# Optimization experiments

Measured on AMD Instinct MI355X. Metric: run time of the kernel, lower is better.

## Reference

```python
import jax, jax.numpy as jnp
import numpy as np

ALPHA = 0.2          # LeakyReLU negative slope
NEG_CAP = -9e15      # clamp used by the original torch.where on log(adj)


def setup_inputs() -> dict:
    key = jax.random.key(0)
    B, C, V, L, H, E = 4, 32, 1000, 12, 4, 20000
    k1, k2, k3, k4 = jax.random.split(key, 4)
    x = jax.random.normal(k1, (B, C, V, L), dtype=jnp.float32)
    # xavier_uniform-like scale with gain 1.414 (use normal for simplicity of stats)
    W = jax.random.normal(k2, (H, C, C), dtype=jnp.float32) * np.float32(1.414 * np.sqrt(2.0 / (C + C)))
    a = jax.random.normal(k3, (H, 2 * C, 1), dtype=jnp.float32) * np.float32(1.414 * np.sqrt(2.0 / (2 * C + 1)))
    # edge list: V self-loops (every row nonempty -> rowsum > 0) + random edges
    rng = np.random.default_rng(0)
    src = np.concatenate([np.arange(V), rng.integers(0, V, E - V)]).astype(np.int64)
    dst = np.concatenate([np.arange(V), rng.integers(0, V, E - V)]).astype(np.int64)
    edge_index = jnp.asarray(np.stack([src, dst]))           # [2, E]
    # edge_val = adj[edge0, edge1]; positive so log() is finite
    edge_val = jax.random.uniform(k4, (E,), dtype=jnp.float32, minval=0.05, maxval=1.0)
    return {"x": x, "W": W, "a": a, "edge_index": edge_index, "edge_val": edge_val}


def reference(x, W, a, edge_index, edge_val):
    # x: [B,C,V,L], W: [H,C,C], a: [H,2C,1], edge_index: [2,E], edge_val: [E]
    H, C = W.shape[0], W.shape[2]
    V = x.shape[2]
    e0, e1 = edge_index[0], edge_index[1]

    # h = einsum('ncvl,hcd->hndvl'): [H,B,C,V,L]
    h = jnp.einsum('bcvl,hcd->hbdvl', x, W)

    # attention score: a applied to cat(h[src], h[dst]) == a_src.h[src] + a_dst.h[dst]
    a_src, a_dst = a[:, :C, 0], a[:, C:, 0]                   # [H,C]
    s_src = jnp.einsum('hbcvl,hc->hbvl', h, a_src)            # [H,B,V,L]
    s_dst = jnp.einsum('hbcvl,hc->hbvl', h, a_dst)
    score = s_src[:, :, e0, :] + s_dst[:, :, e1, :]           # [H,B,E,L]

    edge_e = jnp.exp(-jax.nn.leaky_relu(score, ALPHA))        # [H,B,E,L]
    lv = jnp.maximum(jnp.log(edge_val), NEG_CAP)              # [E]
    edge_e = edge_e * lv[None, None, :, None]
    # (dropout is identity in eval mode)

    # e_rowsum: sparse [V,V] @ ones -> per-row sum, scatter by e0: [V,H,B,L]
    rowsum = jax.ops.segment_sum(jnp.moveaxis(edge_e, 2, 0), e0, num_segments=V)

    # h_prime numerator: scatter (edge_e * h[dst]) by e0
    hg = h[:, :, :, e1, :]                                    # [H,B,C,E,L]
    msg = edge_e[:, :, None, :, :] * hg                       # [H,B,C,E,L]
    num = jax.ops.segment_sum(jnp.moveaxis(msg, 3, 0), e0, num_segments=V)  # [V,H,B,C,L]

    h_prime = num / rowsum[:, :, :, None, :]                  # [V,H,B,C,L]
    h_avg = jnp.mean(h_prime, axis=1)                         # [V,B,C,L]
    out = jnp.transpose(h_avg, (1, 2, 0, 3))                  # [B,C,V,L]
    return jax.nn.elu(out)
```

## Files before the change

### kernel.cpp

```cpp
#include <hip/hip_runtime.h>
#include <hip/hip_bf16.h>
#include <math.h>

#define HH 4
#define BB 4
#define CC 32
#define VV 1000
#define LL 12
#define EE 20000
#define NBL (BB * LL)
#define SS (HH * NBL)
#define RCAP 128
#define LALPHA 0.2f
#define NEG_CAP_F -9000000000000000.0f

typedef unsigned int uint;
typedef unsigned short ushort;

__global__ __launch_bounds__(256) void k_h(const float* __restrict__ x,
                                           const float* __restrict__ W,
                                           const float* __restrict__ a,
                                           ushort* __restrict__ h_g,
                                           float* __restrict__ s_src,
                                           float* __restrict__ s_dst,
                                           int* __restrict__ cnt) {
  if (blockIdx.y == 0 && blockIdx.x < 4) {
    cnt[blockIdx.x * 256 + threadIdx.x] = 0;
  }

  __shared__ float W_lds[HH * CC * CC];
  __shared__ float a_lds[HH * 2 * CC];
  __shared__ float x_lds[CC * 8 * LL];
  __shared__ float wa[HH][2][CC];
  const int tid = threadIdx.x;
  const int b = blockIdx.y;
  const int v0 = blockIdx.x * 8;

  for (int i = tid; i < HH * CC * CC; i += 256) W_lds[i] = W[i];
  a_lds[tid] = a[tid];
  for (int i = tid; i < CC * 8 * LL; i += 256) {
    int ci = i / (8 * LL);
    int r = i - ci * (8 * LL);
    x_lds[i] = x[(b * CC + ci) * (VV * LL) + v0 * LL + r];
  }
  __syncthreads();

  {
    int h = tid >> 6, rest = tid & 63, which = rest >> 5, ci = rest & 31;
    float acc = 0.f;
#pragma unroll
    for (int c = 0; c < CC; ++c)
      acc = fmaf(W_lds[h * CC * CC + ci * CC + c],
                 a_lds[h * 2 * CC + which * CC + c], acc);
    wa[h][which][ci] = acc;
  }
  __syncthreads();

  const int vp = tid >> 5;
  const int c = tid & 31;

  float acc[HH][LL];
#pragma unroll
  for (int h = 0; h < HH; ++h)
#pragma unroll
    for (int l = 0; l < LL; ++l) acc[h][l] = 0.f;

#pragma unroll 4
  for (int ci = 0; ci < CC; ++ci) {
    float xv[LL];
#pragma unroll
    for (int l = 0; l < LL; ++l) xv[l] = x_lds[ci * 96 + vp * LL + l];
#pragma unroll
    for (int h = 0; h < HH; ++h) {
      float w = W_lds[h * CC * CC + ci * CC + c];
#pragma unroll
      for (int l = 0; l < LL; ++l) acc[h][l] = fmaf(xv[l], w, acc[h][l]);
    }
  }

  const int v = v0 + vp;
#pragma unroll
  for (int h = 0; h < HH; ++h)
#pragma unroll
    for (int l = 0; l < LL; ++l) {
      int slab = h * NBL + b * LL + l;
      __hip_bfloat16 bf = __float2bfloat16(acc[h][l]);
      h_g[((size_t)slab * VV + v) * CC + c] = *(ushort*)&bf;
    }

  {
    int q = tid & 31;
    int vp2 = tid >> 5;
    for (int cb = q; cb < HH * LL; cb += 32) {
      int h = cb / LL, l = cb - (cb / LL) * LL;
      float as = 0.f, ad = 0.f;
#pragma unroll
      for (int ci = 0; ci < CC; ++ci) {
        float xr = x_lds[ci * 96 + vp2 * LL + l];
        as = fmaf(xr, wa[h][0][ci], as);
        ad = fmaf(xr, wa[h][1][ci], ad);
      }
      int slab = h * NBL + b * LL + l;
      s_src[slab * VV + v0 + vp2] = as;
      s_dst[slab * VV + v0 + vp2] = ad;
    }
  }
}

__global__ __launch_bounds__(256) void k_scatter(const int* __restrict__ ei,
                                                 const float* __restrict__ ev,
                                                 int* __restrict__ cnt,
                                                 uint2* __restrict__ csr) {
  int e = blockIdx.x * 256 + threadIdx.x;
  if (e >= EE) return;
  int r = ei[e];
  int d = ei[EE + e];
  int pos = atomicAdd(&cnt[r], 1);
  if (pos < RCAP) {
    float lv = fmaxf(__logf(ev[e]), NEG_CAP_F);
    csr[r * RCAP + pos] = make_uint2((uint)d, __float_as_uint(lv));
  }
}

__global__ __launch_bounds__(256) void k_agg(const ushort* __restrict__ hg,
                                             const float* __restrict__ s_src,
                                             const float* __restrict__ s_dst,
                                             const int* __restrict__ cnt,
                                             const uint2* __restrict__ csr,
                                             float* __restrict__ outp) {
  __shared__ uint2 ed[4][2][HH][16];
  const int i = blockIdx.x;
  const int xcd = i & 7;
  const int q = i >> 3;
  const int bl = xcd * 6 + q / 250;
  const int vb = q % 250;
  const int warp = threadIdx.x >> 6;
  const int v = vb * 4 + warp;
  const int lane = threadIdx.x & 63;
  const int b = bl / LL, l = bl - b * LL;

  int deg = cnt[v];
  if (deg > RCAP) deg = RCAP;
  const int rbase = v * RCAP;

  const int ha = lane >> 4;
  const int ia = lane & 15;
  const int slabA = ha * NBL + bl;
  const float ssv = s_src[slabA * VV + v];
  const float* sdbA = s_dst + slabA * VV;

  const int jj = lane >> 5;
  const int c = lane & 31;

  float num[HH] = {0.f, 0.f, 0.f, 0.f};
  float rs[HH] = {0.f, 0.f, 0.f, 0.f};
  const ushort* hgs[HH];
#pragma unroll
  for (int h = 0; h < HH; ++h)
    hgs[h] = hg + (size_t)(h * NBL + bl) * (VV * CC);

  for (int base = 0; base < deg; base += 16) {
    const int par = (base >> 4) & 1;
    int e = base + ia;
    float eev = 0.f;
    int d = 0;
    if (e < deg) {
      uint2 ent = csr[rbase + e];
      d = (int)ent.x;
      float lv = __uint_as_float(ent.y);
      float s = ssv + sdbA[d];
      float lr = s > 0.f ? s : LALPHA * s;
      eev = __expf(-lr) * lv;
    }
    ed[warp][par][ha][ia] = make_uint2((uint)d, __float_as_uint(eev));

    int m = deg - base;
    if (m > 16) m = 16;
    int iters = (m + 1) >> 1;
    for (int t = 0; t < iters; ++t) {
      int idx = t * 2 + jj;
#pragma unroll
      for (int h = 0; h < HH; ++h) {
        uint2 p = ed[warp][par][h][idx];
        float e2 = __uint_as_float(p.y);
        ushort gv = hgs[h][p.x * CC + c];
        num[h] = fmaf(e2, __uint_as_float((uint)gv << 16), num[h]);
        rs[h] += e2;
      }
    }
  }

  float acc = 0.f;
#pragma unroll
  for (int h = 0; h < HH; ++h) {
    float n = num[h] + __shfl_xor(num[h], 32);
    float r = rs[h] + __shfl_xor(rs[h], 32);
    acc += __fdividef(n, r);
  }
  if (jj == 0) {
    float mv = acc * 0.25f;
    float res = mv > 0.f ? mv : expm1f(mv);
    outp[((size_t)(b * CC + c) * VV + v) * LL + l] = res;
  }
}

extern "C" void kernel_launch(void* const* d_in, const int* in_sizes, int n_in,
                              void* d_out, int out_size, void* d_ws, size_t ws_size,
                              hipStream_t stream) {
  const float* x = (const float*)d_in[0];
  const float* W = (const float*)d_in[1];
  const float* a = (const float*)d_in[2];
  const int* ei = (const int*)d_in[3];
  const float* ev = (const float*)d_in[4];
  float* out = (float*)d_out;
  float* ws = (float*)d_ws;

  size_t o = 0;
  ushort* h_g = (ushort*)(ws + o);  o += (size_t)SS * VV * CC / 2;
  float* s_src = ws + o;            o += SS * VV;
  float* s_dst = ws + o;            o += SS * VV;
  int* cnt = (int*)(ws + o);        o += 1024;
  uint2* csr = (uint2*)(ws + o);    o += (size_t)VV * RCAP * 2;

  dim3 gA(VV / 8, BB);
  k_h<<<gA, 256, 0, stream>>>(x, W, a, h_g, s_src, s_dst, cnt);

  k_scatter<<<(EE + 255) / 256, 256, 0, stream>>>(ei, ev, cnt, csr);

  const int nblk = NBL * (VV / 4);
  k_agg<<<nblk, 256, 0, stream>>>(h_g, s_src, s_dst, cnt, csr, out);
}
```

Measured before the change: 69.53 us.

## Split head projection across grid z and widen aggregation gathers to bf16 pairs

The projection kernel now handles two heads per block, with a third grid dimension covering the head pairs. This doubles the block count and cuts per-thread accumulators and LDS use. The aggregation kernel has each lane load a 32-bit word holding two bf16 channels and process four edges in parallel per wavefront. The partial sums are then reduced with two shuffle stages, and per-edge weights for all heads are stored together so one float4 LDS read fetches them. This is meant to halve the gather instruction count and improve occupancy, in exchange for extra shuffle reductions and only a quarter of the lanes doing the final writes.

```diff
diff --git a/kernel.cpp b/kernel.cpp
--- a/kernel.cpp
+++ b/kernel.cpp
@@ -24,20 +24,21 @@
                                            float* __restrict__ s_src,
                                            float* __restrict__ s_dst,
                                            int* __restrict__ cnt) {
-  if (blockIdx.y == 0 && blockIdx.x < 4) {
+  const int hp = blockIdx.z;
+  if (hp == 0 && blockIdx.y == 0 && blockIdx.x < 4) {
     cnt[blockIdx.x * 256 + threadIdx.x] = 0;
   }
 
-  __shared__ float W_lds[HH * CC * CC];
-  __shared__ float a_lds[HH * 2 * CC];
+  __shared__ float W_lds[2 * CC * CC];
+  __shared__ float a_lds[2 * 2 * CC];
   __shared__ float x_lds[CC * 8 * LL];
-  __shared__ float wa[HH][2][CC];
+  __shared__ float wa[2][2][CC];
   const int tid = threadIdx.x;
   const int b = blockIdx.y;
   const int v0 = blockIdx.x * 8;
 
-  for (int i = tid; i < HH * CC * CC; i += 256) W_lds[i] = W[i];
-  a_lds[tid] = a[tid];
+  for (int i = tid; i < 2 * CC * CC; i += 256) W_lds[i] = W[hp * 2 * CC * CC + i];
+  if (tid < 128) a_lds[tid] = a[hp * 128 + tid];
   for (int i = tid; i < CC * 8 * LL; i += 256) {
     int ci = i / (8 * LL);
     int r = i - ci * (8 * LL);
@@ -45,25 +46,27 @@
   }
   __syncthreads();
 
-  {
-    int h = tid >> 6, rest = tid & 63, which = rest >> 5, ci = rest & 31;
+  if (tid < 128) {
+    int hh = tid >> 6, rest = tid & 63, which = rest >> 5, ci = rest & 31;
     float acc = 0.f;
 #pragma unroll
-    for (int c = 0; c < CC; ++c)
-      acc = fmaf(W_lds[h * CC * CC + ci * CC + c],
-                 a_lds[h * 2 * CC + which * CC + c], acc);
-    wa[h][which][ci] = acc;
+    for (int k = 0; k < CC; ++k) {
+      int c = (k + ci) & 31;
+      acc = fmaf(W_lds[hh * CC * CC + ci * CC + c],
+                 a_lds[hh * 2 * CC + which * CC + c], acc);
+    }
+    wa[hh][which][ci] = acc;
   }
   __syncthreads();
 
   const int vp = tid >> 5;
   const int c = tid & 31;
 
-  float acc[HH][LL];
-#pragma unroll
-  for (int h = 0; h < HH; ++h)
-#pragma unroll
-    for (int l = 0; l < LL; ++l) acc[h][l] = 0.f;
+  float acc[2][LL];
+#pragma unroll
+  for (int hh = 0; hh < 2; ++hh)
+#pragma unroll
+    for (int l = 0; l < LL; ++l) acc[hh][l] = 0.f;
 
 #pragma unroll 4
   for (int ci = 0; ci < CC; ++ci) {
@@ -71,36 +74,36 @@
 #pragma unroll
     for (int l = 0; l < LL; ++l) xv[l] = x_lds[ci * 96 + vp * LL + l];
 #pragma unroll
-    for (int h = 0; h < HH; ++h) {
-      float w = W_lds[h * CC * CC + ci * CC + c];
-#pragma unroll
-      for (int l = 0; l < LL; ++l) acc[h][l] = fmaf(xv[l], w, acc[h][l]);
+    for (int hh = 0; hh < 2; ++hh) {
+      float w = W_lds[hh * CC * CC + ci * CC + c];
+#pragma unroll
+      for (int l = 0; l < LL; ++l) acc[hh][l] = fmaf(xv[l], w, acc[hh][l]);
     }
   }
 
   const int v = v0 + vp;
 #pragma unroll
-  for (int h = 0; h < HH; ++h)
+  for (int hh = 0; hh < 2; ++hh)
 #pragma unroll
     for (int l = 0; l < LL; ++l) {
-      int slab = h * NBL + b * LL + l;
-      __hip_bfloat16 bf = __float2bfloat16(acc[h][l]);
+      int slab = (hp * 2 + hh) * NBL + b * LL + l;
+      __hip_bfloat16 bf = __float2bfloat16(acc[hh][l]);
       h_g[((size_t)slab * VV + v) * CC + c] = *(ushort*)&bf;
     }
 
   {
     int q = tid & 31;
     int vp2 = tid >> 5;
-    for (int cb = q; cb < HH * LL; cb += 32) {
-      int h = cb / LL, l = cb - (cb / LL) * LL;
+    if (q < 24) {
+      int hh = q / LL, l = q - (q / LL) * LL;
       float as = 0.f, ad = 0.f;
 #pragma unroll
       for (int ci = 0; ci < CC; ++ci) {
         float xr = x_lds[ci * 96 + vp2 * LL + l];
-        as = fmaf(xr, wa[h][0][ci], as);
-        ad = fmaf(xr, wa[h][1][ci], ad);
+        as = fmaf(xr, wa[hh][0][ci], as);
+        ad = fmaf(xr, wa[hh][1][ci], ad);
       }
-      int slab = h * NBL + b * LL + l;
+      int slab = (hp * 2 + hh) * NBL + b * LL + l;
       s_src[slab * VV + v0 + vp2] = as;
       s_dst[slab * VV + v0 + vp2] = ad;
     }
@@ -128,7 +131,8 @@
                                              const int* __restrict__ cnt,
                                              const uint2* __restrict__ csr,
                                              float* __restrict__ outp) {
-  __shared__ uint2 ed[4][2][HH][16];
+  __shared__ uint ed_dst[4][2][16];
+  __shared__ float ed_ee[4][2][16][HH];
   const int i = blockIdx.x;
   const int xcd = i & 7;
   const int q = i >> 3;
@@ -149,15 +153,19 @@
   const float ssv = s_src[slabA * VV + v];
   const float* sdbA = s_dst + slabA * VV;
 
-  const int jj = lane >> 5;
-  const int c = lane & 31;
-
-  float num[HH] = {0.f, 0.f, 0.f, 0.f};
-  float rs[HH] = {0.f, 0.f, 0.f, 0.f};
-  const ushort* hgs[HH];
+  const int ii = lane >> 4;
+  const int cq = lane & 15;
+
+  float num[HH][2];
+  float rs[HH];
+#pragma unroll
+  for (int h = 0; h < HH; ++h) {
+    num[h][0] = 0.f; num[h][1] = 0.f; rs[h] = 0.f;
+  }
+  const uint* hgs[HH];
 #pragma unroll
   for (int h = 0; h < HH; ++h)
-    hgs[h] = hg + (size_t)(h * NBL + bl) * (VV * CC);
+    hgs[h] = (const uint*)(hg + (size_t)(h * NBL + bl) * (VV * CC));
 
   for (int base = 0; base < deg; base += 16) {
     const int par = (base >> 4) & 1;
@@ -172,35 +180,52 @@
       float lr = s > 0.f ? s : LALPHA * s;
       eev = __expf(-lr) * lv;
     }
-    ed[warp][par][ha][ia] = make_uint2((uint)d, __float_as_uint(eev));
+    ed_ee[warp][par][ia][ha] = eev;
+    if (ha == 0) ed_dst[warp][par][ia] = (uint)d;
 
     int m = deg - base;
     if (m > 16) m = 16;
-    int iters = (m + 1) >> 1;
+    int iters = (m + 3) >> 2;
     for (int t = 0; t < iters; ++t) {
-      int idx = t * 2 + jj;
+      int idx = t * 4 + ii;
+      uint d2 = ed_dst[warp][par][idx];
+      const float4 e4 = *(const float4*)&ed_ee[warp][par][idx][0];
+      const uint cix = d2 * (CC / 2) + cq;
 #pragma unroll
       for (int h = 0; h < HH; ++h) {
-        uint2 p = ed[warp][par][h][idx];
-        float e2 = __uint_as_float(p.y);
-        ushort gv = hgs[h][p.x * CC + c];
-        num[h] = fmaf(e2, __uint_as_float((uint)gv << 16), num[h]);
-        rs[h] += e2;
+        float eh = (h == 0) ? e4.x : (h == 1) ? e4.y : (h == 2) ? e4.z : e4.w;
+        uint g = hgs[h][cix];
+        num[h][0] = fmaf(eh, __uint_as_float(g << 16), num[h][0]);
+        num[h][1] = fmaf(eh, __uint_as_float(g & 0xffff0000u), num[h][1]);
+        rs[h] += eh;
       }
     }
   }
 
-  float acc = 0.f;
-#pragma unroll
-  for (int h = 0; h < HH; ++h) {
-    float n = num[h] + __shfl_xor(num[h], 32);
-    float r = rs[h] + __shfl_xor(rs[h], 32);
-    acc += __fdividef(n, r);
-  }
-  if (jj == 0) {
-    float mv = acc * 0.25f;
-    float res = mv > 0.f ? mv : expm1f(mv);
-    outp[((size_t)(b * CC + c) * VV + v) * LL + l] = res;
+#pragma unroll
+  for (int m = 16; m <= 32; m <<= 1) {
+#pragma unroll
+    for (int h = 0; h < HH; ++h) {
+      num[h][0] += __shfl_xor(num[h][0], m);
+      num[h][1] += __shfl_xor(num[h][1], m);
+      rs[h] += __shfl_xor(rs[h], m);
+    }
+  }
+
+  if (ii == 0) {
+    float a0 = 0.f, a1 = 0.f;
+#pragma unroll
+    for (int h = 0; h < HH; ++h) {
+      float inv = __frcp_rn(rs[h]);
+      a0 = fmaf(num[h][0], inv, a0);
+      a1 = fmaf(num[h][1], inv, a1);
+    }
+    a0 *= 0.25f; a1 *= 0.25f;
+    a0 = a0 > 0.f ? a0 : expm1f(a0);
+    a1 = a1 > 0.f ? a1 : expm1f(a1);
+    size_t o0 = ((size_t)(b * CC + 2 * cq) * VV + v) * LL + l;
+    outp[o0] = a0;
+    outp[o0 + (size_t)VV * LL] = a1;
   }
 }
 
@@ -222,7 +247,7 @@
   int* cnt = (int*)(ws + o);        o += 1024;
   uint2* csr = (uint2*)(ws + o);    o += (size_t)VV * RCAP * 2;
 
-  dim3 gA(VV / 8, BB);
+  dim3 gA(VV / 8, BB, 2);
   k_h<<<gA, 256, 0, stream>>>(x, W, a, h_g, s_src, s_dst, cnt);
 
   k_scatter<<<(EE + 255) / 256, 256, 0, stream>>>(ei, ev, cnt, csr);
```

After: 65.86 us. 5.3% less time.

## Vectorize bf16 gathers in aggregation and repartition projection kernel threads

Applied to the files above, without the earlier changes.

The aggregation kernel now has each lane load a uint4 holding eight bf16 channels per neighbor, with lanes split across heads, channel groups and four edges at a time. Results are combined with cross-lane shuffles and a reciprocal before the ELU output. This replaces many 2-byte scalar gathers with fewer wide loads. The projection kernel now uses 2 vertices per block and one head per thread group, reads x directly from global memory, loads W with float4, and computes s_src/s_dst with a simpler thread mapping. The trade-offs are more blocks redundantly loading W and a more complex reduction.

```diff
diff --git a/kernel.cpp b/kernel.cpp
--- a/kernel.cpp
+++ b/kernel.cpp
@@ -30,80 +30,80 @@
 
   __shared__ float W_lds[HH * CC * CC];
   __shared__ float a_lds[HH * 2 * CC];
-  __shared__ float x_lds[CC * 8 * LL];
+  __shared__ float x_s[CC * 2 * LL];
   __shared__ float wa[HH][2][CC];
   const int tid = threadIdx.x;
   const int b = blockIdx.y;
-  const int v0 = blockIdx.x * 8;
-
-  for (int i = tid; i < HH * CC * CC; i += 256) W_lds[i] = W[i];
+  const int v0 = blockIdx.x * 2;
+
+  {
+    const float4* Wf = (const float4*)W;
+    float4* Wl = (float4*)W_lds;
+    for (int i = tid; i < HH * CC * CC / 4; i += 256) Wl[i] = Wf[i];
+  }
   a_lds[tid] = a[tid];
-  for (int i = tid; i < CC * 8 * LL; i += 256) {
-    int ci = i / (8 * LL);
-    int r = i - ci * (8 * LL);
-    x_lds[i] = x[(b * CC + ci) * (VV * LL) + v0 * LL + r];
+#pragma unroll
+  for (int k = 0; k < 3; ++k) {
+    int i = k * 256 + tid;
+    int ci = i / 24, r = i - ci * 24;
+    x_s[i] = x[(b * CC + ci) * (VV * LL) + v0 * LL + r];
   }
   __syncthreads();
 
   {
-    int h = tid >> 6, rest = tid & 63, which = rest >> 5, ci = rest & 31;
+    int h = tid >> 6, which = (tid >> 5) & 1, ci = tid & 31;
     float acc = 0.f;
 #pragma unroll
-    for (int c = 0; c < CC; ++c)
+    for (int k = 0; k < CC; ++k) {
+      int c = (k + ci) & 31;
       acc = fmaf(W_lds[h * CC * CC + ci * CC + c],
                  a_lds[h * 2 * CC + which * CC + c], acc);
+    }
     wa[h][which][ci] = acc;
   }
   __syncthreads();
 
-  const int vp = tid >> 5;
+  const int vp = tid >> 7;
+  const int h = (tid >> 5) & 3;
   const int c = tid & 31;
-
-  float acc[HH][LL];
-#pragma unroll
-  for (int h = 0; h < HH; ++h)
-#pragma unroll
-    for (int l = 0; l < LL; ++l) acc[h][l] = 0.f;
+  const int v = v0 + vp;
+
+  int xoff = (b * CC) * (VV * LL) + v * LL;
+  xoff = __builtin_amdgcn_readfirstlane(xoff);
+  const float* xr = x + xoff;
+
+  float acc[LL];
+#pragma unroll
+  for (int l = 0; l < LL; ++l) acc[l] = 0.f;
 
 #pragma unroll 4
   for (int ci = 0; ci < CC; ++ci) {
-    float xv[LL];
-#pragma unroll
-    for (int l = 0; l < LL; ++l) xv[l] = x_lds[ci * 96 + vp * LL + l];
-#pragma unroll
-    for (int h = 0; h < HH; ++h) {
-      float w = W_lds[h * CC * CC + ci * CC + c];
-#pragma unroll
-      for (int l = 0; l < LL; ++l) acc[h][l] = fmaf(xv[l], w, acc[h][l]);
-    }
-  }
-
-  const int v = v0 + vp;
-#pragma unroll
-  for (int h = 0; h < HH; ++h)
-#pragma unroll
-    for (int l = 0; l < LL; ++l) {
-      int slab = h * NBL + b * LL + l;
-      __hip_bfloat16 bf = __float2bfloat16(acc[h][l]);
-      h_g[((size_t)slab * VV + v) * CC + c] = *(ushort*)&bf;
-    }
-
-  {
-    int q = tid & 31;
-    int vp2 = tid >> 5;
-    for (int cb = q; cb < HH * LL; cb += 32) {
-      int h = cb / LL, l = cb - (cb / LL) * LL;
-      float as = 0.f, ad = 0.f;
-#pragma unroll
-      for (int ci = 0; ci < CC; ++ci) {
-        float xr = x_lds[ci * 96 + vp2 * LL + l];
-        as = fmaf(xr, wa[h][0][ci], as);
-        ad = fmaf(xr, wa[h][1][ci], ad);
-      }
-      int slab = h * NBL + b * LL + l;
-      s_src[slab * VV + v0 + vp2] = as;
-      s_dst[slab * VV + v0 + vp2] = ad;
-    }
+    float w = W_lds[h * CC * CC + ci * CC + c];
+#pragma unroll
+    for (int l = 0; l < LL; ++l)
+      acc[l] = fmaf(xr[ci * (VV * LL) + l], w, acc[l]);
+  }
+
+  const int slab0 = h * NBL + b * LL;
+#pragma unroll
+  for (int l = 0; l < LL; ++l) {
+    __hip_bfloat16 bf = __float2bfloat16(acc[l]);
+    h_g[((size_t)(slab0 + l) * VV + v) * CC + c] = *(ushort*)&bf;
+  }
+
+  if (tid < 192) {
+    int which = tid & 1;
+    int t2 = tid >> 1;
+    int l = t2 % 12;
+    int h2 = (t2 / 12) & 3;
+    int vp2 = t2 / 48;
+    float s = 0.f;
+#pragma unroll
+    for (int ci = 0; ci < CC; ++ci)
+      s = fmaf(x_s[ci * 24 + vp2 * 12 + l], wa[h2][which][ci], s);
+    int slab = h2 * NBL + b * LL + l;
+    float* dp = which ? s_dst : s_src;
+    dp[slab * VV + v0 + vp2] = s;
   }
 }
 
@@ -128,7 +128,8 @@
                                              const int* __restrict__ cnt,
                                              const uint2* __restrict__ csr,
                                              float* __restrict__ outp) {
-  __shared__ uint2 ed[4][2][HH][16];
+  __shared__ uint ed_dst[4][16];
+  __shared__ float ed_ee[4][16][HH];
   const int i = blockIdx.x;
   const int xcd = i & 7;
   const int q = i >> 3;
@@ -149,18 +150,18 @@
   const float ssv = s_src[slabA * VV + v];
   const float* sdbA = s_dst + slabA * VV;
 
-  const int jj = lane >> 5;
-  const int c = lane & 31;
-
-  float num[HH] = {0.f, 0.f, 0.f, 0.f};
-  float rs[HH] = {0.f, 0.f, 0.f, 0.f};
-  const ushort* hgs[HH];
-#pragma unroll
-  for (int h = 0; h < HH; ++h)
-    hgs[h] = hg + (size_t)(h * NBL + bl) * (VV * CC);
+  const int ii = lane >> 4;
+  const int h = (lane >> 2) & 3;
+  const int cg = lane & 3;
+
+  const uint4* hgl = (const uint4*)(hg + (size_t)(h * NBL + bl) * (VV * CC));
+
+  float num[8];
+#pragma unroll
+  for (int j = 0; j < 8; ++j) num[j] = 0.f;
+  float rs = 0.f;
 
   for (int base = 0; base < deg; base += 16) {
-    const int par = (base >> 4) & 1;
     int e = base + ia;
     float eev = 0.f;
     int d = 0;
@@ -172,35 +173,54 @@
       float lr = s > 0.f ? s : LALPHA * s;
       eev = __expf(-lr) * lv;
     }
-    ed[warp][par][ha][ia] = make_uint2((uint)d, __float_as_uint(eev));
+    ed_ee[warp][ia][ha] = eev;
+    if (ha == 0) ed_dst[warp][ia] = (uint)d;
 
     int m = deg - base;
     if (m > 16) m = 16;
-    int iters = (m + 1) >> 1;
+    int iters = (m + 3) >> 2;
     for (int t = 0; t < iters; ++t) {
-      int idx = t * 2 + jj;
-#pragma unroll
-      for (int h = 0; h < HH; ++h) {
-        uint2 p = ed[warp][par][h][idx];
-        float e2 = __uint_as_float(p.y);
-        ushort gv = hgs[h][p.x * CC + c];
-        num[h] = fmaf(e2, __uint_as_float((uint)gv << 16), num[h]);
-        rs[h] += e2;
-      }
+      int idx = (t << 2) + ii;
+      uint d2 = ed_dst[warp][idx];
+      float eh = ed_ee[warp][idx][h];
+      uint4 g = hgl[d2 * 4 + cg];
+      num[0] = fmaf(eh, __uint_as_float(g.x << 16), num[0]);
+      num[1] = fmaf(eh, __uint_as_float(g.x & 0xffff0000u), num[1]);
+      num[2] = fmaf(eh, __uint_as_float(g.y << 16), num[2]);
+      num[3] = fmaf(eh, __uint_as_float(g.y & 0xffff0000u), num[3]);
+      num[4] = fmaf(eh, __uint_as_float(g.z << 16), num[4]);
+      num[5] = fmaf(eh, __uint_as_float(g.z & 0xffff0000u), num[5]);
+      num[6] = fmaf(eh, __uint_as_float(g.w << 16), num[6]);
+      num[7] = fmaf(eh, __uint_as_float(g.w & 0xffff0000u), num[7]);
+      rs += eh;
     }
   }
 
-  float acc = 0.f;
-#pragma unroll
-  for (int h = 0; h < HH; ++h) {
-    float n = num[h] + __shfl_xor(num[h], 32);
-    float r = rs[h] + __shfl_xor(rs[h], 32);
-    acc += __fdividef(n, r);
-  }
-  if (jj == 0) {
-    float mv = acc * 0.25f;
-    float res = mv > 0.f ? mv : expm1f(mv);
-    outp[((size_t)(b * CC + c) * VV + v) * LL + l] = res;
+#pragma unroll
+  for (int mm = 16; mm <= 32; mm <<= 1) {
+#pragma unroll
+    for (int j = 0; j < 8; ++j) num[j] += __shfl_xor(num[j], mm);
+    rs += __shfl_xor(rs, mm);
+  }
+  float inv = __frcp_rn(rs);
+  float val[8];
+#pragma unroll
+  for (int j = 0; j < 8; ++j) val[j] = num[j] * inv;
+#pragma unroll
+  for (int mm = 4; mm <= 8; mm <<= 1) {
+#pragma unroll
+    for (int j = 0; j < 8; ++j) val[j] += __shfl_xor(val[j], mm);
+  }
+
+  if (ii == 0) {
+    int j0 = 2 * h;
+    float a0 = val[j0] * 0.25f;
+    float a1 = val[j0 + 1] * 0.25f;
+    a0 = a0 > 0.f ? a0 : expm1f(a0);
+    a1 = a1 > 0.f ? a1 : expm1f(a1);
+    size_t o0 = ((size_t)(b * CC + cg * 8 + j0) * VV + v) * LL + l;
+    outp[o0] = a0;
+    outp[o0 + (size_t)VV * LL] = a1;
   }
 }
 
@@ -222,7 +242,7 @@
   int* cnt = (int*)(ws + o);        o += 1024;
   uint2* csr = (uint2*)(ws + o);    o += (size_t)VV * RCAP * 2;
 
-  dim3 gA(VV / 8, BB);
+  dim3 gA(VV / 2, BB);
   k_h<<<gA, 256, 0, stream>>>(x, W, a, h_g, s_src, s_dst, cnt);
 
   k_scatter<<<(EE + 255) / 256, 256, 0, stream>>>(ei, ev, cnt, csr);
```

After: 61.05 us. 12.2% less time.
